# Performance work log

Hardware: AMD Instinct MI355X
Metric: run time of the kernel (lower is better)

## Reference

```python
import jax, jax.numpy as jnp
import numpy as np

D_IN = 768
D_OUT = 768
NUM_HEADS = 12
HEAD_DIM = D_OUT // NUM_HEADS


def setup_inputs() -> dict:
    key = jax.random.key(0)
    ks = jax.random.split(key, 6)
    s = 0.02
    x = jax.random.normal(ks[0], (2, 4096, D_IN), dtype=jnp.float32)
    w_query = jax.random.normal(ks[1], (D_IN, D_OUT), dtype=jnp.float32) * s
    w_key = jax.random.normal(ks[2], (D_IN, D_OUT), dtype=jnp.float32) * s
    w_value = jax.random.normal(ks[3], (D_IN, D_OUT), dtype=jnp.float32) * s
    w_out = jax.random.normal(ks[4], (D_OUT, D_OUT), dtype=jnp.float32) * s
    b_out = jnp.zeros((D_OUT,), dtype=jnp.float32)
    return {"x": x, "w_query": w_query, "w_key": w_key, "w_value": w_value,
            "w_out": w_out, "b_out": b_out}


def reference(x, w_query, w_key, w_value, w_out, b_out):
    b, n, _ = x.shape
    # projections -> [b, n, h, d]
    q = (x @ w_query).reshape(b, n, NUM_HEADS, HEAD_DIM)
    k = (x @ w_key).reshape(b, n, NUM_HEADS, HEAD_DIM)
    v = (x @ w_value).reshape(b, n, NUM_HEADS, HEAD_DIM)
    # scores [b, h, q, k]
    scores = jnp.einsum('bqhd,bkhd->bhqk', q, k)
    causal = jnp.triu(jnp.ones((n, n), dtype=bool), k=1)  # True above diagonal
    scores = jnp.where(causal, -jnp.inf, scores)
    scale = 1.0 / jnp.sqrt(jnp.asarray(HEAD_DIM, dtype=scores.dtype))
    weights = jax.nn.softmax(scores * scale, axis=-1)
    # dropout p=0.0 -> identity
    ctx = jnp.einsum('bhqk,bkhd->bqhd', weights, v).reshape(b, n, D_OUT)
    return ctx @ w_out + b_out
```

## Files before the change

### kernel.cpp

```cpp
#include <hip/hip_runtime.h>

typedef unsigned short ushort_t;
typedef __bf16 bf16_t;
typedef float floatx4 __attribute__((ext_vector_type(4)));
typedef bf16_t bf16x8 __attribute__((ext_vector_type(8)));
typedef float f32x4 __attribute__((ext_vector_type(4)));
typedef unsigned short u16x4 __attribute__((ext_vector_type(4)));
typedef unsigned short u16x8 __attribute__((ext_vector_type(8)));
typedef unsigned int u32x2 __attribute__((ext_vector_type(2)));

#define NTOK 4096
#define NHEAD 12
#define HD 64
#define DMODEL 768
#define NROWS 8192
#define NBH 24

__device__ __forceinline__ ushort_t f2bf(float f) {
  union { float f; unsigned u; } v; v.f = f;
  unsigned u = v.u;
  unsigned r = u + 0x7fffu + ((u >> 16) & 1u);
  return (ushort_t)(r >> 16);
}

__device__ __forceinline__ float bf2f(ushort_t s) {
  union { unsigned u; float f; } v; v.u = (unsigned)s << 16; return v.f;
}

__device__ __forceinline__ void async16(const void* g, void* l) {
  __builtin_amdgcn_global_load_lds(
      (const __attribute__((address_space(1))) void*)g,
      (__attribute__((address_space(3))) void*)l, 16, 0, 0);
}


__global__ __launch_bounds__(256) void transpose_w4(
    const float* __restrict__ s0, const float* __restrict__ s1,
    const float* __restrict__ s2, const float* __restrict__ s3,
    ushort_t* __restrict__ d_qkv, ushort_t* __restrict__ d_o) {
  __shared__ float t[32][33];
  const int m = blockIdx.z;
  const float* src = (m == 0) ? s0 : (m == 1) ? s1 : (m == 2) ? s2 : s3;
  ushort_t* dst = (m < 3) ? (d_qkv + (size_t)m * DMODEL * DMODEL) : d_o;
  const int bi = blockIdx.x, bj = blockIdx.y;
  const int r = threadIdx.x >> 5, c = threadIdx.x & 31;
  for (int p = 0; p < 4; ++p)
    t[r + p * 8][c] = src[(size_t)(bi * 32 + r + p * 8) * DMODEL + bj * 32 + c];
  __syncthreads();
  for (int p = 0; p < 4; ++p)
    dst[(size_t)(bj * 32 + r + p * 8) * DMODEL + bi * 32 + c] = f2bf(t[c][r + p * 8]);
}

__global__ void convert_x(const float* __restrict__ in, ushort_t* __restrict__ out) {
  int idx = blockIdx.x * 256 + threadIdx.x;
  f32x4 v = ((const f32x4*)in)[idx];
  u16x4 o;
  o.x = f2bf(v.x); o.y = f2bf(v.y); o.z = f2bf(v.z); o.w = f2bf(v.w);
  ((u16x4*)out)[idx] = o;
}

__global__ __launch_bounds__(256) void gemm_bt(
    const ushort_t* __restrict__ A, const ushort_t* __restrict__ B, int K, int mode,
    ushort_t* __restrict__ q_ws, ushort_t* __restrict__ k_ws, ushort_t* __restrict__ v_ws,
    float* __restrict__ outF, const float* __restrict__ bias,
    const ushort_t* __restrict__ opart, const float* __restrict__ lpart) {
  __shared__ __align__(16) ushort_t a_lds[128 * 32];
  __shared__ __align__(16) ushort_t b_lds[128 * 32];
  const int tid = threadIdx.x;
  const int w = tid >> 6, lane = tid & 63;
  const int quad = lane >> 4, l16 = lane & 15;
  const int wm = w >> 1, wn = w & 1;
  const size_t row0 = (size_t)blockIdx.x * 128;
  const size_t col0 = (size_t)blockIdx.y * 128;

  const int srow = w * 32 + (lane >> 2);
  const int kbyte = (lane & 3) * 16;
  const char* aG = (const char*)(A + (row0 + srow) * (size_t)K) + kbyte;
  const char* bG = (const char*)(B + (col0 + srow) * (size_t)K) + kbyte;
  const size_t rstep = (size_t)16 * K * 2;
  char* aL = (char*)a_lds + (size_t)(w * 2) * 1024;
  char* bL = (char*)b_lds + (size_t)(w * 2) * 1024;

  floatx4 acc[4][4];
  for (int i = 0; i < 4; ++i)
    for (int j = 0; j < 4; ++j) acc[i][j] = (floatx4){0.f, 0.f, 0.f, 0.f};

  const int nk = K / 32;
  for (int kt = 0; kt < nk; ++kt) {
    const size_t koff = (size_t)kt * 64;
    __syncthreads();
    if (mode == 2) {
      const int col = kt * 32 + (lane & 3) * 8;
      const int h = col >> 6, dd = col & 63;
#pragma unroll
      for (int sl = 0; sl < 2; ++sl) {
        int row = (int)row0 + srow + sl * 16;
        int b = row >> 12, n = row & 4095;
        int bh = b * NHEAD + h;
        size_t i0 = ((size_t)bh * NTOK + n) * HD + dd;
        size_t i1 = i0 + (size_t)NBH * NTOK * HD;
        u16x8 a = *(const u16x8*)&opart[i0];
        u16x8 c = *(const u16x8*)&opart[i1];
        float inv = 1.0f / (lpart[(size_t)bh * NTOK + n] + lpart[(size_t)(NBH + bh) * NTOK + n]);
        u16x8 o;
#pragma unroll
        for (int j = 0; j < 8; ++j) o[j] = f2bf((bf2f(a[j]) + bf2f(c[j])) * inv);
        *(u16x8*)(aL + sl * 1024 + (size_t)lane * 16) = o;
      }
    } else {
      async16(aG + koff, aL);
      async16(aG + koff + rstep, aL + 1024);
    }
    async16(bG + koff, bL);
    async16(bG + koff + rstep, bL + 1024);
    __syncthreads();
    bf16x8 af[4], bfr[4];
    for (int mt = 0; mt < 4; ++mt)
      af[mt] = *(bf16x8*)&a_lds[(wm * 64 + mt * 16 + l16) * 32 + quad * 8];
    for (int nt = 0; nt < 4; ++nt)
      bfr[nt] = *(bf16x8*)&b_lds[(wn * 64 + nt * 16 + l16) * 32 + quad * 8];
    for (int mt = 0; mt < 4; ++mt)
      for (int nt = 0; nt < 4; ++nt)
        acc[mt][nt] = __builtin_amdgcn_mfma_f32_16x16x32_bf16(af[mt], bfr[nt], acc[mt][nt], 0, 0, 0);
  }

  if (mode == 0) {
    const int which = (int)(col0 / DMODEL);
    if (which < 2) {
      ushort_t* dstT = (which == 0) ? q_ws : k_ws;
      const float scale = (which == 0) ? 0.125f * 1.4426950408889634f : 1.0f;
      for (int mt = 0; mt < 4; ++mt) {
        int gr = (int)row0 + wm * 64 + mt * 16 + quad * 4;
        int b = gr >> 12;
        int n0 = gr & 4095;
        for (int nt = 0; nt < 4; ++nt) {
          int gc = (int)col0 + wn * 64 + nt * 16 + l16;
          int cc = gc - which * DMODEL;
          int h = cc >> 6, d = cc & 63;
          size_t base = ((size_t)(b * NHEAD + h) * NTOK + n0) * HD + d;
          for (int r = 0; r < 4; ++r)
            dstT[base + (size_t)r * HD] = f2bf(acc[mt][nt][r] * scale);
        }
      }
    } else {
      for (int mt = 0; mt < 4; ++mt) {
        int gr = (int)row0 + wm * 64 + mt * 16 + quad * 4;
        int b = gr >> 12;
        int n0 = gr & 4095;
        for (int nt = 0; nt < 4; ++nt) {
          int gc = (int)col0 + wn * 64 + nt * 16 + l16;
          int cc = gc - 2 * DMODEL;
          int h = cc >> 6, d = cc & 63;
          u16x4 ov;
          for (int r = 0; r < 4; ++r) ov[r] = f2bf(acc[mt][nt][r]);
          unsigned d0 = ((unsigned*)&ov)[0], d1 = ((unsigned*)&ov)[1];
          unsigned p0 = (unsigned)__shfl_xor((int)d0, 16);
          unsigned p1 = (unsigned)__shfl_xor((int)d1, 16);
          if (!(quad & 1)) {
            u16x8 pk;
            ((unsigned*)&pk)[0] = d0; ((unsigned*)&pk)[1] = d1;
            ((unsigned*)&pk)[2] = p0; ((unsigned*)&pk)[3] = p1;
            *(u16x8*)&v_ws[((size_t)(b * NHEAD + h) * HD + d) * NTOK + n0] = pk;
          }
        }
      }
    }
  } else {
    for (int mt = 0; mt < 4; ++mt) {
      int gr = (int)row0 + wm * 64 + mt * 16 + quad * 4;
      for (int nt = 0; nt < 4; ++nt) {
        int gc = (int)col0 + wn * 64 + nt * 16 + l16;
        float bv = bias[gc];
        for (int r = 0; r < 4; ++r)
          outF[(size_t)(gr + r) * DMODEL + gc] = acc[mt][nt][r] + bv;
      }
    }
  }
}

__global__ __launch_bounds__(128, 2) void attn6(
    const ushort_t* __restrict__ Qh, const ushort_t* __restrict__ Kh,
    const ushort_t* __restrict__ Vt, ushort_t* __restrict__ o_part,
    float* __restrict__ l_part) {
  __shared__ __align__(16) ushort_t k_lds[2][8 * 512];
  __shared__ __align__(16) ushort_t v_lds[2][8 * 512];
  __shared__ __align__(16) ushort_t q_lds[16 * 512];
  const int tid = threadIdx.x;
  const int w = tid >> 6, lane = tid & 63;
  const int quad = lane >> 4, l16 = lane & 15;
  const int bh = blockIdx.x;
  const int split = blockIdx.z;
  const size_t hbase = (size_t)bh * NTOK * HD;
  const ushort_t* Qb = Qh + hbase;
  const ushort_t* Kb = Kh + hbase;
  const ushort_t* Vb = Vt + hbase;
  const size_t obase = ((size_t)split * NBH + bh) * NTOK * HD;
  const size_t lbase = ((size_t)split * NBH + bh) * NTOK;

  for (int phase = 0; phase < 2; ++phase) {
    const int qt = (phase == 0) ? (int)blockIdx.y : 31 - (int)blockIdx.y;
    const int Q0 = qt * 128;
    const int nkt = 2 * qt + 2;
    const int kt_lo = (split == 0) ? 0 : nkt / 2;
    const int kt_hi = (split == 0) ? nkt / 2 : nkt;
    const int nit = kt_hi - kt_lo;
    __syncthreads();
#pragma unroll
    for (int i = 0; i < 8; ++i) {
      int s = w * 8 + i;
      async16(Qb + (size_t)(Q0 + w * 64 + (i >> 1) * 16 + l16) * HD + (i & 1) * 32 + quad * 8,
              (char*)q_lds + s * 1024);
    }
    {
      const int k0p = kt_lo * 64;
#pragma unroll
      for (int i = 0; i < 4; ++i) {
        int s = w * 4 + i;
        async16(Kb + (size_t)(k0p + (s >> 1) * 16 + l16) * HD + (s & 1) * 32 + quad * 8,
                (char*)k_lds + s * 1024);
        async16(Vb + (size_t)((s >> 1) * 16 + l16) * NTOK + k0p + (s & 1) * 32 + quad * 8,
                (char*)v_lds + s * 1024);
      }
    }
    __asm volatile("s_waitcnt vmcnt(0)" ::: "memory");
    bf16x8 qr[4][2];
#pragma unroll
    for (int qf = 0; qf < 4; ++qf)
#pragma unroll
      for (int hh = 0; hh < 2; ++hh)
        qr[qf][hh] = *(const bf16x8*)((const char*)q_lds + ((w * 8 + qf * 2 + hh) * 1024) + lane * 16);

    floatx4 o[4][4];
    float lp[4] = {0.f, 0.f, 0.f, 0.f};
#pragma unroll
    for (int qf = 0; qf < 4; ++qf)
#pragma unroll
      for (int dt = 0; dt < 4; ++dt) o[qf][dt] = (floatx4){0.f, 0.f, 0.f, 0.f};

    const int wq0 = Q0 + w * 64;

    for (int it = 0; it < nit; ++it) {
      const int kt = kt_lo + it;
      const int cur = it & 1;
      __syncthreads();
      if (it + 1 < nit) {
        const int k1 = (kt + 1) * 64;
#pragma unroll
        for (int i = 0; i < 4; ++i) {
          int s = w * 4 + i;
          async16(Kb + (size_t)(k1 + (s >> 1) * 16 + l16) * HD + (s & 1) * 32 + quad * 8,
                  (char*)k_lds + (cur ^ 1) * 8192 + s * 1024);
          async16(Vb + (size_t)((s >> 1) * 16 + l16) * NTOK + k1 + (s & 1) * 32 + quad * 8,
                  (char*)v_lds + (cur ^ 1) * 8192 + s * 1024);
        }
      }
      const int k0 = kt * 64;
      if (k0 > wq0 + 63) continue;
      const char* kb = (const char*)k_lds + cur * 8192;
      const char* vb = (const char*)v_lds + cur * 8192;
      const bool need_mask = (k0 + 63 > wq0);

#pragma unroll
      for (int half = 0; half < 2; ++half) {
        floatx4 st[4][2];
#pragma unroll
        for (int m2 = 0; m2 < 2; ++m2) {
          const int mt = half * 2 + m2;
          bf16x8 kf0 = *(const bf16x8*)(kb + (mt * 2 + 0) * 1024 + lane * 16);
          bf16x8 kf1 = *(const bf16x8*)(kb + (mt * 2 + 1) * 1024 + lane * 16);
#pragma unroll
          for (int qf = 0; qf < 4; ++qf) {
            floatx4 z = (floatx4){0.f, 0.f, 0.f, 0.f};
            z = __builtin_amdgcn_mfma_f32_16x16x32_bf16(kf0, qr[qf][0], z, 0, 0, 0);
            z = __builtin_amdgcn_mfma_f32_16x16x32_bf16(kf1, qr[qf][1], z, 0, 0, 0);
            st[qf][m2] = z;
          }
        }
#pragma unroll
        for (int qf = 0; qf < 4; ++qf) {
          const int qg = wq0 + qf * 16 + l16;
          float sum = 0.f;
#pragma unroll
          for (int m2 = 0; m2 < 2; ++m2) {
            const int mt = half * 2 + m2;
            float p[4];
#pragma unroll
            for (int r = 0; r < 4; ++r) {
              float e = __builtin_exp2f(st[qf][m2][r]);
              if (need_mask && (k0 + mt * 16 + quad * 4 + r > qg)) e = 0.f;
              p[r] = e;
              sum += e;
            }
            union { float f; unsigned u; } c0, c1, c2, c3;
            c0.f = p[0]; c1.f = p[1]; c2.f = p[2]; c3.f = p[3];
            u32x2 pk;
            pk.x = __builtin_amdgcn_perm(c1.u, c0.u, 0x07060302u);
            pk.y = __builtin_amdgcn_perm(c3.u, c2.u, 0x07060302u);
            char* dst = (char*)q_lds + ((w * 8 + qf * 2 + (mt >> 1)) * 1024)
                        + ((((mt & 1) * 2 + (quad >> 1)) * 16 + l16) * 16) + (quad & 1) * 8;
            *(u32x2*)dst = pk;
          }
          lp[qf] += sum;
        }
      }
      __asm volatile("s_waitcnt lgkmcnt(0)" ::: "memory");
      bf16x8 pf[4][2];
#pragma unroll
      for (int qf = 0; qf < 4; ++qf)
#pragma unroll
        for (int hh = 0; hh < 2; ++hh)
          pf[qf][hh] = *(const bf16x8*)((const char*)q_lds + ((w * 8 + qf * 2 + hh) * 1024) + lane * 16);
#pragma unroll
      for (int dt = 0; dt < 4; ++dt) {
        bf16x8 vf0 = *(const bf16x8*)(vb + (dt * 2 + 0) * 1024 + lane * 16);
        bf16x8 vf1 = *(const bf16x8*)(vb + (dt * 2 + 1) * 1024 + lane * 16);
#pragma unroll
        for (int qf = 0; qf < 4; ++qf) {
          o[qf][dt] = __builtin_amdgcn_mfma_f32_16x16x32_bf16(pf[qf][0], vf0, o[qf][dt], 0, 0, 0);
          o[qf][dt] = __builtin_amdgcn_mfma_f32_16x16x32_bf16(pf[qf][1], vf1, o[qf][dt], 0, 0, 0);
        }
      }
    }

#pragma unroll
    for (int qf = 0; qf < 4; ++qf) {
      float lf = lp[qf];
      lf += __shfl_xor(lf, 16);
      lf += __shfl_xor(lf, 32);
#pragma unroll
      for (int r = 0; r < 4; ++r) {
        float lq = __shfl(lf, quad * 4 + r);
        int qg = wq0 + qf * 16 + quad * 4 + r;
        size_t base = obase + (size_t)qg * HD;
#pragma unroll
        for (int dt = 0; dt < 4; ++dt)
          o_part[base + dt * 16 + l16] = f2bf(o[qf][dt][r]);
        if (l16 == 0) l_part[lbase + qg] = lq;
      }
    }
  }
}

extern "C" void kernel_launch(void* const* d_in, const int* in_sizes, int n_in,
                              void* d_out, int out_size, void* d_ws, size_t ws_size,
                              hipStream_t stream) {
  const float* x  = (const float*)d_in[0];
  const float* wq = (const float*)d_in[1];
  const float* wk = (const float*)d_in[2];
  const float* wv = (const float*)d_in[3];
  const float* wo = (const float*)d_in[4];
  const float* bo = (const float*)d_in[5];
  float* out = (float*)d_out;

  ushort_t* ws = (ushort_t*)d_ws;
  ushort_t* wqkvT = ws;
  ushort_t* woutT = wqkvT + 2304 * 768;
  ushort_t* xbf   = woutT + 768 * 768;
  ushort_t* qh    = xbf + (size_t)NROWS * DMODEL;
  ushort_t* kh    = qh + (size_t)NBH * NTOK * HD;
  ushort_t* vt    = kh + (size_t)NBH * NTOK * HD;
  ushort_t* opart = vt + (size_t)NBH * NTOK * HD;
  float*    lpart = (float*)(opart + (size_t)2 * NBH * NTOK * HD);

  transpose_w4<<<dim3(24, 24, 4), 256, 0, stream>>>(wq, wk, wv, wo, wqkvT, woutT);
  convert_x<<<6144, 256, 0, stream>>>(x, xbf);

  gemm_bt<<<dim3(64, 18), 256, 0, stream>>>(xbf, wqkvT, DMODEL, 0,
                                            qh, kh, vt, nullptr, nullptr, nullptr, nullptr);
  attn6<<<dim3(24, 16, 2), 128, 0, stream>>>(qh, kh, vt, opart, lpart);
  gemm_bt<<<dim3(64, 6), 256, 0, stream>>>(opart, woutT, DMODEL, 2,
                                           nullptr, nullptr, nullptr, out, bo, opart, lpart);
}
```

Measured before the change: 313.0 us.

## Keep softmax probabilities in registers and widen attention blocks to four waves

The attention kernel now runs 256 threads (4 waves of 32 query rows) instead of 2 waves of 64 rows. The softmax probabilities no longer round-trip through LDS: the QK MFMA output layout is fed directly as the A operand of 16x16x16 bf16 MFMAs for PV. V tiles are loaded with a swizzled layout to match that operand layout. Q is staged in the unused second halves of the K/V double buffers, which drops the separate Q LDS buffer. This removes LDS write/read traffic and waits for P and cuts registers per wave, but it uses the smaller-K MFMA and doubles the number of PV MFMA issues.

```diff
diff --git a/kernel.cpp b/kernel.cpp
--- a/kernel.cpp
+++ b/kernel.cpp
@@ -4,6 +4,8 @@
 typedef __bf16 bf16_t;
 typedef float floatx4 __attribute__((ext_vector_type(4)));
 typedef bf16_t bf16x8 __attribute__((ext_vector_type(8)));
+typedef bf16_t bf16x4 __attribute__((ext_vector_type(4)));
+typedef short s16x4 __attribute__((ext_vector_type(4)));
 typedef float f32x4 __attribute__((ext_vector_type(4)));
 typedef unsigned short u16x4 __attribute__((ext_vector_type(4)));
 typedef unsigned short u16x8 __attribute__((ext_vector_type(8)));
@@ -31,6 +33,24 @@
   __builtin_amdgcn_global_load_lds(
       (const __attribute__((address_space(1))) void*)g,
       (__attribute__((address_space(3))) void*)l, 16, 0, 0);
+}
+
+__device__ __forceinline__ floatx4 mfma16(unsigned a0, unsigned a1,
+                                          unsigned b0, unsigned b1, floatx4 c) {
+#if defined(__HIP_DEVICE_COMPILE__)
+#if __has_builtin(__builtin_amdgcn_mfma_f32_16x16x16_bf16)
+  union { unsigned u[2]; bf16x4 v; } A, B;
+  A.u[0] = a0; A.u[1] = a1; B.u[0] = b0; B.u[1] = b1;
+  return __builtin_amdgcn_mfma_f32_16x16x16_bf16(A.v, B.v, c, 0, 0, 0);
+#else
+  union { unsigned u[2]; s16x4 v; } A, B;
+  A.u[0] = a0; A.u[1] = a1; B.u[0] = b0; B.u[1] = b1;
+  return __builtin_amdgcn_mfma_f32_16x16x16bf16_1k(A.v, B.v, c, 0, 0, 0);
+#endif
+#else
+  (void)a0; (void)a1; (void)b0; (void)b1;
+  return c;
+#endif
 }
 
 
@@ -178,13 +198,12 @@
   }
 }
 
-__global__ __launch_bounds__(128, 2) void attn6(
+__global__ __launch_bounds__(256) void attn7(
     const ushort_t* __restrict__ Qh, const ushort_t* __restrict__ Kh,
     const ushort_t* __restrict__ Vt, ushort_t* __restrict__ o_part,
     float* __restrict__ l_part) {
   __shared__ __align__(16) ushort_t k_lds[2][8 * 512];
   __shared__ __align__(16) ushort_t v_lds[2][8 * 512];
-  __shared__ __align__(16) ushort_t q_lds[16 * 512];
   const int tid = threadIdx.x;
   const int w = tid >> 6, lane = tid & 63;
   const int quad = lane >> 4, l16 = lane & 15;
@@ -197,47 +216,51 @@
   const size_t obase = ((size_t)split * NBH + bh) * NTOK * HD;
   const size_t lbase = ((size_t)split * NBH + bh) * NTOK;
 
+  const int vrow = lane >> 3;
+  const int vc = lane & 7;
+  const int vkoff = ((2 * vc + 16 - 4 * (vrow & 3)) & 15) * 4;
+  const int psw = quad + 4 * (l16 & 3);
+
   for (int phase = 0; phase < 2; ++phase) {
     const int qt = (phase == 0) ? (int)blockIdx.y : 31 - (int)blockIdx.y;
     const int Q0 = qt * 128;
     const int nkt = 2 * qt + 2;
     const int kt_lo = (split == 0) ? 0 : nkt / 2;
-    const int kt_hi = (split == 0) ? nkt / 2 : nkt;
-    const int nit = kt_hi - kt_lo;
+    const int nit = nkt / 2;
     __syncthreads();
-#pragma unroll
-    for (int i = 0; i < 8; ++i) {
-      int s = w * 8 + i;
-      async16(Qb + (size_t)(Q0 + w * 64 + (i >> 1) * 16 + l16) * HD + (i & 1) * 32 + quad * 8,
-              (char*)q_lds + s * 1024);
-    }
+    char* qstage = (w < 2) ? ((char*)k_lds + 8192 + w * 4096)
+                           : ((char*)v_lds + 8192 + (w - 2) * 4096);
+#pragma unroll
+    for (int i = 0; i < 4; ++i)
+      async16(Qb + (size_t)(Q0 + w * 32 + (i >> 1) * 16 + l16) * HD + (i & 1) * 32 + quad * 8,
+              qstage + i * 1024);
     {
       const int k0p = kt_lo * 64;
 #pragma unroll
-      for (int i = 0; i < 4; ++i) {
-        int s = w * 4 + i;
+      for (int i = 0; i < 2; ++i) {
+        int s = w * 2 + i;
         async16(Kb + (size_t)(k0p + (s >> 1) * 16 + l16) * HD + (s & 1) * 32 + quad * 8,
                 (char*)k_lds + s * 1024);
-        async16(Vb + (size_t)((s >> 1) * 16 + l16) * NTOK + k0p + (s & 1) * 32 + quad * 8,
+        async16(Vb + (size_t)(s * 8 + vrow) * NTOK + k0p + vkoff,
                 (char*)v_lds + s * 1024);
       }
     }
     __asm volatile("s_waitcnt vmcnt(0)" ::: "memory");
-    bf16x8 qr[4][2];
-#pragma unroll
-    for (int qf = 0; qf < 4; ++qf)
+    bf16x8 qr[2][2];
+#pragma unroll
+    for (int qf = 0; qf < 2; ++qf)
 #pragma unroll
       for (int hh = 0; hh < 2; ++hh)
-        qr[qf][hh] = *(const bf16x8*)((const char*)q_lds + ((w * 8 + qf * 2 + hh) * 1024) + lane * 16);
-
-    floatx4 o[4][4];
-    float lp[4] = {0.f, 0.f, 0.f, 0.f};
-#pragma unroll
-    for (int qf = 0; qf < 4; ++qf)
+        qr[qf][hh] = *(const bf16x8*)(qstage + (qf * 2 + hh) * 1024 + lane * 16);
+
+    floatx4 o[2][4];
+    float lp[2] = {0.f, 0.f};
+#pragma unroll
+    for (int qf = 0; qf < 2; ++qf)
 #pragma unroll
       for (int dt = 0; dt < 4; ++dt) o[qf][dt] = (floatx4){0.f, 0.f, 0.f, 0.f};
 
-    const int wq0 = Q0 + w * 64;
+    const int wq0 = Q0 + w * 32;
 
     for (int it = 0; it < nit; ++it) {
       const int kt = kt_lo + it;
@@ -246,84 +269,60 @@
       if (it + 1 < nit) {
         const int k1 = (kt + 1) * 64;
 #pragma unroll
-        for (int i = 0; i < 4; ++i) {
-          int s = w * 4 + i;
+        for (int i = 0; i < 2; ++i) {
+          int s = w * 2 + i;
           async16(Kb + (size_t)(k1 + (s >> 1) * 16 + l16) * HD + (s & 1) * 32 + quad * 8,
                   (char*)k_lds + (cur ^ 1) * 8192 + s * 1024);
-          async16(Vb + (size_t)((s >> 1) * 16 + l16) * NTOK + k1 + (s & 1) * 32 + quad * 8,
+          async16(Vb + (size_t)(s * 8 + vrow) * NTOK + k1 + vkoff,
                   (char*)v_lds + (cur ^ 1) * 8192 + s * 1024);
         }
       }
       const int k0 = kt * 64;
-      if (k0 > wq0 + 63) continue;
+      if (k0 > wq0 + 31) continue;
       const char* kb = (const char*)k_lds + cur * 8192;
       const char* vb = (const char*)v_lds + cur * 8192;
       const bool need_mask = (k0 + 63 > wq0);
 
 #pragma unroll
-      for (int half = 0; half < 2; ++half) {
-        floatx4 st[4][2];
-#pragma unroll
-        for (int m2 = 0; m2 < 2; ++m2) {
-          const int mt = half * 2 + m2;
-          bf16x8 kf0 = *(const bf16x8*)(kb + (mt * 2 + 0) * 1024 + lane * 16);
-          bf16x8 kf1 = *(const bf16x8*)(kb + (mt * 2 + 1) * 1024 + lane * 16);
-#pragma unroll
-          for (int qf = 0; qf < 4; ++qf) {
-            floatx4 z = (floatx4){0.f, 0.f, 0.f, 0.f};
-            z = __builtin_amdgcn_mfma_f32_16x16x32_bf16(kf0, qr[qf][0], z, 0, 0, 0);
-            z = __builtin_amdgcn_mfma_f32_16x16x32_bf16(kf1, qr[qf][1], z, 0, 0, 0);
-            st[qf][m2] = z;
+      for (int g = 0; g < 4; ++g) {
+        bf16x8 kf0 = *(const bf16x8*)(kb + (g * 2 + 0) * 1024 + lane * 16);
+        bf16x8 kf1 = *(const bf16x8*)(kb + (g * 2 + 1) * 1024 + lane * 16);
+        floatx4 z0 = (floatx4){0.f, 0.f, 0.f, 0.f};
+        floatx4 z1 = (floatx4){0.f, 0.f, 0.f, 0.f};
+        z0 = __builtin_amdgcn_mfma_f32_16x16x32_bf16(kf0, qr[0][0], z0, 0, 0, 0);
+        z1 = __builtin_amdgcn_mfma_f32_16x16x32_bf16(kf0, qr[1][0], z1, 0, 0, 0);
+        z0 = __builtin_amdgcn_mfma_f32_16x16x32_bf16(kf1, qr[0][1], z0, 0, 0, 0);
+        z1 = __builtin_amdgcn_mfma_f32_16x16x32_bf16(kf1, qr[1][1], z1, 0, 0, 0);
+        unsigned pa[2][2];
+#pragma unroll
+        for (int qf = 0; qf < 2; ++qf) {
+          floatx4 z = qf ? z1 : z0;
+          float p[4];
+          const int qg = wq0 + qf * 16 + l16;
+#pragma unroll
+          for (int r = 0; r < 4; ++r) {
+            float e = __builtin_exp2f(z[r]);
+            if (need_mask && (k0 + g * 16 + quad * 4 + r > qg)) e = 0.f;
+            p[r] = e;
           }
-        }
-#pragma unroll
-        for (int qf = 0; qf < 4; ++qf) {
-          const int qg = wq0 + qf * 16 + l16;
-          float sum = 0.f;
-#pragma unroll
-          for (int m2 = 0; m2 < 2; ++m2) {
-            const int mt = half * 2 + m2;
-            float p[4];
-#pragma unroll
-            for (int r = 0; r < 4; ++r) {
-              float e = __builtin_exp2f(st[qf][m2][r]);
-              if (need_mask && (k0 + mt * 16 + quad * 4 + r > qg)) e = 0.f;
-              p[r] = e;
-              sum += e;
-            }
-            union { float f; unsigned u; } c0, c1, c2, c3;
-            c0.f = p[0]; c1.f = p[1]; c2.f = p[2]; c3.f = p[3];
-            u32x2 pk;
-            pk.x = __builtin_amdgcn_perm(c1.u, c0.u, 0x07060302u);
-            pk.y = __builtin_amdgcn_perm(c3.u, c2.u, 0x07060302u);
-            char* dst = (char*)q_lds + ((w * 8 + qf * 2 + (mt >> 1)) * 1024)
-                        + ((((mt & 1) * 2 + (quad >> 1)) * 16 + l16) * 16) + (quad & 1) * 8;
-            *(u32x2*)dst = pk;
-          }
-          lp[qf] += sum;
-        }
-      }
-      __asm volatile("s_waitcnt lgkmcnt(0)" ::: "memory");
-      bf16x8 pf[4][2];
-#pragma unroll
-      for (int qf = 0; qf < 4; ++qf)
-#pragma unroll
-        for (int hh = 0; hh < 2; ++hh)
-          pf[qf][hh] = *(const bf16x8*)((const char*)q_lds + ((w * 8 + qf * 2 + hh) * 1024) + lane * 16);
-#pragma unroll
-      for (int dt = 0; dt < 4; ++dt) {
-        bf16x8 vf0 = *(const bf16x8*)(vb + (dt * 2 + 0) * 1024 + lane * 16);
-        bf16x8 vf1 = *(const bf16x8*)(vb + (dt * 2 + 1) * 1024 + lane * 16);
-#pragma unroll
-        for (int qf = 0; qf < 4; ++qf) {
-          o[qf][dt] = __builtin_amdgcn_mfma_f32_16x16x32_bf16(pf[qf][0], vf0, o[qf][dt], 0, 0, 0);
-          o[qf][dt] = __builtin_amdgcn_mfma_f32_16x16x32_bf16(pf[qf][1], vf1, o[qf][dt], 0, 0, 0);
-        }
-      }
-    }
-
-#pragma unroll
-    for (int qf = 0; qf < 4; ++qf) {
+          lp[qf] += (p[0] + p[1]) + (p[2] + p[3]);
+          union { float f; unsigned u; } c0, c1, c2, c3;
+          c0.f = p[0]; c1.f = p[1]; c2.f = p[2]; c3.f = p[3];
+          pa[qf][0] = __builtin_amdgcn_perm(c1.u, c0.u, 0x07060302u);
+          pa[qf][1] = __builtin_amdgcn_perm(c3.u, c2.u, 0x07060302u);
+        }
+        const int pofs = ((g * 4 + psw) & 15) * 8;
+#pragma unroll
+        for (int dt = 0; dt < 4; ++dt) {
+          u32x2 vv = *(const u32x2*)(vb + dt * 2048 + l16 * 128 + pofs);
+          o[0][dt] = mfma16(pa[0][0], pa[0][1], vv.x, vv.y, o[0][dt]);
+          o[1][dt] = mfma16(pa[1][0], pa[1][1], vv.x, vv.y, o[1][dt]);
+        }
+      }
+    }
+
+#pragma unroll
+    for (int qf = 0; qf < 2; ++qf) {
       float lf = lp[qf];
       lf += __shfl_xor(lf, 16);
       lf += __shfl_xor(lf, 32);
@@ -367,7 +366,7 @@
 
   gemm_bt<<<dim3(64, 18), 256, 0, stream>>>(xbf, wqkvT, DMODEL, 0,
                                             qh, kh, vt, nullptr, nullptr, nullptr, nullptr);
-  attn6<<<dim3(24, 16, 2), 128, 0, stream>>>(qh, kh, vt, opart, lpart);
+  attn7<<<dim3(24, 16, 2), 256, 0, stream>>>(qh, kh, vt, opart, lpart);
   gemm_bt<<<dim3(64, 6), 256, 0, stream>>>(opart, woutT, DMODEL, 2,
                                            nullptr, nullptr, nullptr, out, bo, opart, lpart);
 }
```

Measured after the change: 282.8 us. 9.6% less time.
